# Optimization experiments

Hardware: AMD Instinct MI355X
Metric: run time of the kernel (lower is better)

## Reference

```python
import jax, jax.numpy as jnp
import numpy as np

N, E, G = 50000, 1600000, 64          # nodes, edges, graphs
NODE_IN, EDGE_IN, HID, L, H = 32, 16, 64, 3, 4
C = HID // H                           # per-head channels (PyG out_channels)


def setup_inputs() -> dict:
    key = jax.random.key(0)
    ks = jax.random.split(key, 12)
    x = jax.random.normal(ks[0], (N, NODE_IN), jnp.float32)
    edge_index = jax.random.randint(ks[1], (2, E), 0, N, jnp.int32)
    edge_attr = jax.random.normal(ks[2], (E, EDGE_IN), jnp.float32)
    batch = jnp.sort(jax.random.randint(ks[3], (N,), 0, G, jnp.int32))
    s = lambda k, shape, fan: jax.random.normal(k, shape, jnp.float32) / np.sqrt(fan)
    Wn = s(ks[4], (NODE_IN, HID), NODE_IN); bn = jnp.zeros((HID,), jnp.float32)
    Wq = s(ks[5], (L, HID, HID), HID);      bq = jnp.zeros((L, HID), jnp.float32)
    Wk = s(ks[6], (L, HID, HID), HID);      bk = jnp.zeros((L, HID), jnp.float32)
    Wv = s(ks[7], (L, HID, HID), HID);      bv = jnp.zeros((L, HID), jnp.float32)
    We = s(ks[8], (L, EDGE_IN, HID), EDGE_IN)          # lin_edge, bias=False in PyG
    Ws = s(ks[9], (L, HID, HID), HID);      bs = jnp.zeros((L, HID), jnp.float32)  # lin_skip
    W1 = s(ks[10], (HID, HID // 2), HID);   b1 = jnp.zeros((HID // 2,), jnp.float32)
    W2 = s(ks[11], (HID // 2, 1), HID // 2); b2 = jnp.zeros((1,), jnp.float32)
    return dict(x=x, edge_index=edge_index, edge_attr=edge_attr, batch=batch,
                Wn=Wn, bn=bn, Wq=Wq, bq=bq, Wk=Wk, bk=bk, Wv=Wv, bv=bv,
                We=We, Ws=Ws, bs=bs, W1=W1, b1=b1, W2=W2, b2=b2)


def _transformer_conv(x, src, dst, edge_attr, Wq, bq, Wk, bk, Wv, bv, We, Ws, bs):
    # PyG TransformerConv (concat=True, beta=False, root_weight=True), eval mode.
    q = (x @ Wq + bq)[dst].reshape(E, H, C)              # query at target nodes
    e = (edge_attr @ We).reshape(E, H, C)                # edge embedding
    k = (x @ Wk + bk)[src].reshape(E, H, C) + e          # key at source + edge
    alpha = (q * k).sum(-1) / jnp.sqrt(jnp.float32(C))   # [E, H]
    amax = jax.ops.segment_max(alpha, dst, num_segments=N)
    ex = jnp.exp(alpha - amax[dst])
    denom = jax.ops.segment_sum(ex, dst, num_segments=N)
    attn = ex / (denom[dst] + 1e-16)                     # segment softmax over in-edges
    v = (x @ Wv + bv)[src].reshape(E, H, C) + e
    agg = jax.ops.segment_sum((v * attn[..., None]).reshape(E, HID), dst, num_segments=N)
    return agg + x @ Ws + bs                             # skip connection (lin_skip)


def reference(x, edge_index, edge_attr, batch, Wn, bn, Wq, bq, Wk, bk, Wv, bv,
              We, Ws, bs, W1, b1, W2, b2):
    src, dst = edge_index[0], edge_index[1]
    h = jax.nn.relu(x @ Wn + bn)
    for l in range(L):  # dropout is identity in eval mode
        h_new = jax.nn.relu(_transformer_conv(h, src, dst, edge_attr,
                                              Wq[l], bq[l], Wk[l], bk[l],
                                              Wv[l], bv[l], We[l], Ws[l], bs[l]))
        h = h + h_new
    # global_mean_pool
    cnt = jax.ops.segment_sum(jnp.ones((N,), h.dtype), batch, num_segments=G)
    pooled = jax.ops.segment_sum(h, batch, num_segments=G) / jnp.maximum(cnt, 1.0)[:, None]
    out = jax.nn.relu(pooled @ W1 + b1) @ W2 + b2
    return out.squeeze(-1)
```

## Files before the change

### kernel.cpp

```cpp
#include <hip/hip_runtime.h>
#include <hip/hip_fp16.h>
#include <stdint.h>

#define Nn 50000
#define Ee 1600000
#define Gg 64
#define TB 2048
#define NTB ((Ee + TB - 1) / TB)
#define NBK ((Nn + 255) / 256)

typedef _Float16 f16x2 __attribute__((ext_vector_type(2)));
typedef _Float16 f16x4 __attribute__((ext_vector_type(4)));

__device__ __forceinline__ float fdot2f(f16x2 a, f16x2 b, float c) {
#if __has_builtin(__builtin_amdgcn_fdot2)
    return __builtin_amdgcn_fdot2(a, b, c, false);
#else
    return fmaf((float)a[0], (float)b[0], fmaf((float)a[1], (float)b[1], c));
#endif
}

__global__ void k_hist(const int* __restrict__ ei, int* __restrict__ deg) {
    int e = blockIdx.x * blockDim.x + threadIdx.x;
    if (e < Ee) atomicAdd(&deg[ei[Ee + e]], 1);
}

__global__ void k_scan1(const int* __restrict__ deg, int* __restrict__ row_ptr,
                        int* __restrict__ bsum) {
    __shared__ int buf[256];
    int i = blockIdx.x * 256 + threadIdx.x;
    int v = (i < Nn) ? deg[i] : 0;
    buf[threadIdx.x] = v;
    __syncthreads();
    for (int off = 1; off < 256; off <<= 1) {
        int t = (threadIdx.x >= off) ? buf[threadIdx.x - off] : 0;
        __syncthreads();
        buf[threadIdx.x] += t;
        __syncthreads();
    }
    if (i < Nn) row_ptr[i + 1] = buf[threadIdx.x];
    if (threadIdx.x == 255) bsum[blockIdx.x] = buf[255];
}

__global__ void k_scan2(int* __restrict__ bsum, int nb) {
    __shared__ int buf[256];
    int v = (threadIdx.x < nb) ? bsum[threadIdx.x] : 0;
    buf[threadIdx.x] = v;
    __syncthreads();
    for (int off = 1; off < 256; off <<= 1) {
        int t = (threadIdx.x >= off) ? buf[threadIdx.x - off] : 0;
        __syncthreads();
        buf[threadIdx.x] += t;
        __syncthreads();
    }
    if (threadIdx.x < nb) bsum[threadIdx.x] = buf[threadIdx.x];
}

__global__ void k_scan3(int* __restrict__ row_ptr, const int* __restrict__ bsum) {
    int i = blockIdx.x * 256 + threadIdx.x;
    if (i > Nn) return;
    if (i == 0) { row_ptr[0] = 0; return; }
    int b = (i - 1) >> 8;
    if (b > 0) row_ptr[i] += bsum[b - 1];
}

__global__ void k_scatter(const int* __restrict__ ei, int* __restrict__ cursor,
                          int* __restrict__ src_perm, int* __restrict__ eperm) {
    int e = blockIdx.x * blockDim.x + threadIdx.x;
    if (e >= Ee) return;
    int dst = ei[Ee + e];
    int pos = atomicAdd(&cursor[dst], 1);
    src_perm[pos] = ei[e];
    eperm[pos] = e;
}

__global__ void k_easort(const float* __restrict__ ea, const int* __restrict__ eperm,
                         __half* __restrict__ ea_h) {
    long t = (long)blockIdx.x * blockDim.x + threadIdx.x;
    if (t >= (long)Ee * 4) return;
    long idx = t >> 2;
    int e = eperm[idx];
    float4 v = ((const float4*)ea)[(long)e * 4 + (t & 3)];
    __half2 lo = __floats2half2_rn(v.x, v.y);
    __half2 hi = __floats2half2_rn(v.z, v.w);
    ((__half2*)ea_h)[t * 2]     = lo;
    ((__half2*)ea_h)[t * 2 + 1] = hi;
}


__global__ __launch_bounds__(256) void k_cnt(const int* __restrict__ ei,
                                             int* __restrict__ table) {
    __shared__ int hist[NBK];
    for (int i = threadIdx.x; i < NBK; i += 256) hist[i] = 0;
    __syncthreads();
    int e0 = blockIdx.x * TB;
    for (int i = threadIdx.x; i < TB; i += 256) {
        int e = e0 + i;
        if (e >= Ee) break;
        atomicAdd(&hist[ei[Ee + e] >> 8], 1);
    }
    __syncthreads();
    for (int i = threadIdx.x; i < NBK; i += 256)
        table[i * NTB + blockIdx.x] = hist[i];
}

__global__ __launch_bounds__(256) void k_colscan(int* __restrict__ table,
                                                 int* __restrict__ bktsz) {
    __shared__ int buf[1024];
    int c = blockIdx.x;
    for (int k = 0; k < 4; ++k) {
        int i = threadIdx.x + k * 256;
        buf[i] = (i < NTB) ? table[c * NTB + i] : 0;
    }
    __syncthreads();
    for (int off = 1; off < 1024; off <<= 1) {
        int v[4];
        for (int k = 0; k < 4; ++k) {
            int i = threadIdx.x + k * 256;
            v[k] = (i >= off) ? buf[i - off] : 0;
        }
        __syncthreads();
        for (int k = 0; k < 4; ++k) buf[threadIdx.x + k * 256] += v[k];
        __syncthreads();
    }
    for (int k = 0; k < 4; ++k) {
        int i = threadIdx.x + k * 256;
        if (i < NTB) table[c * NTB + i] = i ? buf[i - 1] : 0;
    }
    if (threadIdx.x == 0) bktsz[c] = buf[1023];
}

__global__ __launch_bounds__(256) void k_bktscan(const int* __restrict__ bktsz,
                                                 int* __restrict__ bktbase) {
    __shared__ int buf[256];
    int i = threadIdx.x;
    buf[i] = (i < NBK) ? bktsz[i] : 0;
    __syncthreads();
    for (int off = 1; off < 256; off <<= 1) {
        int v = (i >= off) ? buf[i - off] : 0;
        __syncthreads();
        buf[i] += v;
        __syncthreads();
    }
    if (i == 0) bktbase[0] = 0;
    if (i < NBK) bktbase[i + 1] = buf[i];
}

__global__ __launch_bounds__(256) void k_binfill(const int* __restrict__ ei,
                        const int* __restrict__ table, const int* __restrict__ bktbase,
                        unsigned long long* __restrict__ tmp) {
    __shared__ int off_s[NBK];
    __shared__ int cnt_s[NBK];
    for (int i = threadIdx.x; i < NBK; i += 256) {
        off_s[i] = table[i * NTB + blockIdx.x];
        cnt_s[i] = 0;
    }
    __syncthreads();
    int e0 = blockIdx.x * TB;
    for (int i = threadIdx.x; i < TB; i += 256) {
        int e = e0 + i;
        if (e >= Ee) break;
        int src = ei[e];
        int dst = ei[Ee + e];
        int b = dst >> 8;
        int r = atomicAdd(&cnt_s[b], 1);
        long pos = (long)bktbase[b] + off_s[b] + r;
        tmp[pos] = ((unsigned long long)(unsigned)dst << 37)
                 | ((unsigned long long)(unsigned)src << 21)
                 | (unsigned long long)(unsigned)e;
    }
}

__global__ __launch_bounds__(256) void k_bktB(const unsigned long long* __restrict__ tmp,
                        const int* __restrict__ bktbase, int* __restrict__ row_ptr,
                        unsigned long long* __restrict__ tmp2) {
    __shared__ int cnt[256];
    __shared__ int sc[256];
    __shared__ int lro[256];
    int b = blockIdx.x, tid = threadIdx.x;
    cnt[tid] = 0;
    __syncthreads();
    int s = bktbase[b], t_end = bktbase[b + 1];
    for (int i = s + tid; i < t_end; i += 256)
        atomicAdd(&cnt[(int)(tmp[i] >> 37) & 255], 1);
    __syncthreads();
    sc[tid] = cnt[tid];
    __syncthreads();
    for (int off = 1; off < 256; off <<= 1) {
        int v = (tid >= off) ? sc[tid - off] : 0;
        __syncthreads();
        sc[tid] += v;
        __syncthreads();
    }
    lro[tid] = tid ? sc[tid - 1] : 0;
    cnt[tid] = 0;
    int n = b * 256 + tid;
    if (n < Nn) row_ptr[n] = s + lro[tid];
    if (b == NBK - 1 && tid == 0) row_ptr[Nn] = Ee;
    __syncthreads();
    for (int i = s + tid; i < t_end; i += 256) {
        unsigned long long p = tmp[i];
        int dn = (int)(p >> 37) & 255;
        int r = atomicAdd(&cnt[dn], 1);
        int pos = s + lro[dn] + r;
        tmp2[pos] = (((p >> 21) & 0xFFFFull) << 32) | (p & 0x1FFFFFull);
    }
}

__global__ void k_scatB(const unsigned long long* __restrict__ tmp2,
                        int* __restrict__ src_perm,
                        const float* __restrict__ ea, __half* __restrict__ ea_h) {
    int t = blockIdx.x * blockDim.x + threadIdx.x;
    if (t >= Ee) return;
    unsigned long long p = tmp2[t];
    src_perm[t] = (int)(p >> 32);
    int e = (int)(p & 0xFFFFFFFFull);
    const float4* er = (const float4*)(ea + (size_t)e * 16);
    float4 v0 = er[0], v1 = er[1], v2 = er[2], v3 = er[3];
    __half2 h0 = __floats2half2_rn(v0.x, v0.y), h1 = __floats2half2_rn(v0.z, v0.w);
    __half2 h2 = __floats2half2_rn(v1.x, v1.y), h3 = __floats2half2_rn(v1.z, v1.w);
    __half2 h4 = __floats2half2_rn(v2.x, v2.y), h5 = __floats2half2_rn(v2.z, v2.w);
    __half2 h6 = __floats2half2_rn(v3.x, v3.y), h7 = __floats2half2_rn(v3.z, v3.w);
    uint4 a = make_uint4(*(unsigned*)&h0, *(unsigned*)&h1,
                         *(unsigned*)&h2, *(unsigned*)&h3);
    uint4 bb = make_uint4(*(unsigned*)&h4, *(unsigned*)&h5,
                          *(unsigned*)&h6, *(unsigned*)&h7);
    uint4* o = (uint4*)(ea_h + (size_t)t * 16);
    o[0] = a;
    o[1] = bb;
}

__global__ void k_gbound(const int* __restrict__ batch, int* __restrict__ gstart) {
    int n = blockIdx.x * blockDim.x + threadIdx.x;
    if (n >= Nn) return;
    int b = batch[n];
    if (n == 0) { for (int g = 0; g <= b; ++g) gstart[g] = 0; }
    else { int bp = batch[n - 1]; for (int g = bp + 1; g <= b; ++g) gstart[g] = n; }
    if (n == Nn - 1) { for (int g = b + 1; g <= Gg; ++g) gstart[g] = Nn; }
}

__global__ __launch_bounds__(256) void k_encode(const float* __restrict__ x,
                         const float* __restrict__ Wn,
                         const float* __restrict__ bn, float* __restrict__ h) {
    __shared__ float sx[64 * 32];
    int base = blockIdx.x * 64;
    for (int i = threadIdx.x; i < 512; i += 256) {
        int off = i * 4, row = off >> 5;
        float4 v = (base + row < Nn) ? ((const float4*)(x))[(base * 32 + off) >> 2]
                                     : make_float4(0.f, 0.f, 0.f, 0.f);
        ((float4*)sx)[i] = v;
    }
    __syncthreads();
    int lane = threadIdx.x & 63, wv = threadIdx.x >> 6;
    float acc[16];
    float b = bn[lane];
#pragma unroll
    for (int nn = 0; nn < 16; ++nn) acc[nn] = b;
#pragma unroll 1
    for (int k0 = 0; k0 < 32; k0 += 4) {
        float w0 = Wn[(k0 + 0) * 64 + lane];
        float w1 = Wn[(k0 + 1) * 64 + lane];
        float w2 = Wn[(k0 + 2) * 64 + lane];
        float w3 = Wn[(k0 + 3) * 64 + lane];
#pragma unroll
        for (int nn = 0; nn < 16; ++nn) {
            int row = wv * 16 + nn;
            float4 hv = *(const float4*)&sx[row * 32 + k0];
            acc[nn] = fmaf(hv.x, w0, fmaf(hv.y, w1, fmaf(hv.z, w2, fmaf(hv.w, w3, acc[nn]))));
        }
    }
#pragma unroll
    for (int nn = 0; nn < 16; ++nn) {
        int n = base + wv * 16 + nn;
        if (n < Nn) h[(size_t)n * 64 + lane] = fmaxf(acc[nn], 0.f);
    }
}

__global__ void k_wqm3(const float* __restrict__ Wq_all, const float* __restrict__ bq_all,
                       const float* __restrict__ We_all, float* __restrict__ Wqm3,
                       float* __restrict__ bqm3) {
    int l = blockIdx.x;
    const float* Wq = Wq_all + l * 4096;
    const float* bq = bq_all + l * 64;
    const float* We = We_all + l * 1024;
    float* Wqm = Wqm3 + l * 4096;
    float* bqm = bqm3 + l * 64;
    for (int o = threadIdx.x; o < 64 * 64; o += 256) {
        int j = o >> 6, lp = o & 63, hh = lp >> 4, ii = lp & 15;
        float acc = 0.f;
#pragma unroll
        for (int c = 0; c < 16; ++c)
            acc += Wq[j * 64 + hh * 16 + c] * We[ii * 64 + hh * 16 + c];
        Wqm[o] = acc;
    }
    if (threadIdx.x < 64) {
        int hh = threadIdx.x >> 4, ii = threadIdx.x & 15;
        float acc = 0.f;
#pragma unroll
        for (int c = 0; c < 16; ++c)
            acc += bq[hh * 16 + c] * We[ii * 64 + hh * 16 + c];
        bqm[threadIdx.x] = acc;
    }
}

__global__ void k_pack(const float* __restrict__ Wq, const float* __restrict__ Wk,
                       const float* __restrict__ Wv, const float* __restrict__ Wqm3,
                       const float* __restrict__ Ws, __half* __restrict__ pw) {
    int l = blockIdx.x / 5, m = blockIdx.x % 5;
    const float SC = 0.25f * 1.4426950408889634f;
    const float* src;
    float sc = 1.f;
    if (m == 0)      { src = Wq + l * 4096;   sc = SC; }
    else if (m == 1) { src = Wk + l * 4096; }
    else if (m == 2) { src = Wv + l * 4096; }
    else if (m == 3) { src = Wqm3 + l * 4096; sc = SC; }
    else             { src = Ws + l * 4096; }
    __half* dst = pw + ((size_t)l * 5 + m) * 4096;
    for (int i = threadIdx.x; i < 4096; i += 256) {
        int k = i >> 6, c = i & 63;
        dst[(k >> 1) * 128 + 2 * c + (k & 1)] = __float2half_rn(src[i] * sc);
    }
}

__global__ __launch_bounds__(256) void k_qkvt2(const float* __restrict__ h,
                       const __half* __restrict__ pw,
                       const float* __restrict__ bq, const float* __restrict__ bk,
                       const float* __restrict__ bv, const float* __restrict__ bqm,
                       const float* __restrict__ bs,
                       __half* __restrict__ qn16, __half* __restrict__ kv,
                       __half* __restrict__ tq16, float* __restrict__ sn) {
    __shared__ __half sh[64 * 64];
    int base = blockIdx.x * 64;
    for (int i = threadIdx.x; i < 1024; i += 256) {
        int off = i * 4, row = off >> 6;
        float4 v = (base + row < Nn) ? ((const float4*)(h))[((size_t)base * 64 + off) >> 2]
                                     : make_float4(0.f, 0.f, 0.f, 0.f);
        ((__half2*)sh)[i * 2]     = __floats2half2_rn(v.x, v.y);
        ((__half2*)sh)[i * 2 + 1] = __floats2half2_rn(v.z, v.w);
    }
    __syncthreads();
    int lane = threadIdx.x & 63, wv = threadIdx.x >> 6;
    const float SC = 0.25f * 1.4426950408889634f;
    const __half* Pq = pw;
    const __half* Pk = pw + 4096;
    const __half* Pv = pw + 8192;
    const __half* Pt = pw + 12288;
    const __half* Ps = pw + 16384;
    float aq[16], ak[16], av[16], at[16], as_[16];
    float _bq = bq[lane] * SC, _bk = bk[lane], _bv = bv[lane],
          _bt = bqm[lane] * SC, _bs = bs[lane];
#pragma unroll
    for (int nn = 0; nn < 16; ++nn) {
        aq[nn] = _bq; ak[nn] = _bk; av[nn] = _bv; at[nn] = _bt; as_[nn] = _bs;
    }
#pragma unroll 1
    for (int k0 = 0; k0 < 64; k0 += 4) {
        int pi = (k0 >> 1) * 128 + 2 * lane;
        f16x2 wq0 = *(const f16x2*)(Pq + pi), wq1 = *(const f16x2*)(Pq + pi + 128);
        f16x2 wk0 = *(const f16x2*)(Pk + pi), wk1 = *(const f16x2*)(Pk + pi + 128);
        f16x2 wv0 = *(const f16x2*)(Pv + pi), wv1 = *(const f16x2*)(Pv + pi + 128);
        f16x2 wt0 = *(const f16x2*)(Pt + pi), wt1 = *(const f16x2*)(Pt + pi + 128);
        f16x2 ws0 = *(const f16x2*)(Ps + pi), ws1 = *(const f16x2*)(Ps + pi + 128);
#pragma unroll
        for (int nn = 0; nn < 16; ++nn) {
            int row = wv * 16 + nn;
            f16x4 hv = *(const f16x4*)&sh[row * 64 + k0];
            f16x2 h01 = __builtin_shufflevector(hv, hv, 0, 1);
            f16x2 h23 = __builtin_shufflevector(hv, hv, 2, 3);
            aq[nn]  = fdot2f(h01, wq0, fdot2f(h23, wq1, aq[nn]));
            ak[nn]  = fdot2f(h01, wk0, fdot2f(h23, wk1, ak[nn]));
            av[nn]  = fdot2f(h01, wv0, fdot2f(h23, wv1, av[nn]));
            at[nn]  = fdot2f(h01, wt0, fdot2f(h23, wt1, at[nn]));
            as_[nn] = fdot2f(h01, ws0, fdot2f(h23, ws1, as_[nn]));
        }
    }
#pragma unroll
    for (int nn = 0; nn < 16; ++nn) {
        int n = base + wv * 16 + nn;
        if (n < Nn) {
            size_t o = (size_t)n * 64 + lane;
            qn16[o] = __float2half_rn(aq[nn]);
            tq16[o] = __float2half_rn(at[nn]);
            sn[o] = as_[nn];
            kv[(size_t)n * 128 + lane]      = __float2half_rn(ak[nn]);
            kv[(size_t)n * 128 + 64 + lane] = __float2half_rn(av[nn]);
        }
    }
}

__global__ __launch_bounds__(256) void k_layer5(float* __restrict__ h,
                      const __half* __restrict__ qn16, const __half* __restrict__ kv,
                      const __half* __restrict__ tq16, const float* __restrict__ sn,
                      const int* __restrict__ row_ptr, const int* __restrict__ src_perm,
                      const __half* __restrict__ eah, const float* __restrict__ We) {
    __shared__ float sWe[1024];
    __shared__ float tE[4][64];
    __shared__ float tV[4][64];
    for (int t = threadIdx.x; t < 1024; t += 256) sWe[t] = We[t];
    __syncthreads();
    int lane = threadIdx.x & 63, wv = threadIdx.x >> 6;
    int slot = lane >> 4, sl = lane & 15;
    int hh = lane >> 4;
    const int xoff = 4 * (sl & 3);
#pragma unroll 1
    for (int j = 0; j < 4; ++j) {
        int n = blockIdx.x * 16 + wv * 4 + j;
        if (n >= Nn) break;
        int beg = row_ptr[n], end = row_ptr[n + 1];
        f16x4 qv = *(const f16x4*)(qn16 + (size_t)n * 64 + 4 * sl);
        f16x4 tv = *(const f16x4*)(tq16 + (size_t)n * 64 + 4 * sl);
        f16x2 qa = __builtin_shufflevector(qv, qv, 0, 1);
        f16x2 qb = __builtin_shufflevector(qv, qv, 2, 3);
        f16x2 ta = __builtin_shufflevector(tv, tv, 0, 1);
        f16x2 tb = __builtin_shufflevector(tv, tv, 2, 3);
        float accd = 0.f;
        float4 accv = make_float4(0.f, 0.f, 0.f, 0.f);
        float4 acce = make_float4(0.f, 0.f, 0.f, 0.f);
        for (int idx = beg; idx < end; idx += 8) {
            int e0 = idx + slot, e1 = idx + 4 + slot;
            bool ok0 = e0 < end, ok1 = e1 < end;
            int i0 = ok0 ? e0 : beg, i1 = ok1 ? e1 : beg;
            int s0 = src_perm[i0], s1 = src_perm[i1];
            f16x4 k0 = *(const f16x4*)(kv + (size_t)s0 * 128 + 4 * sl);
            f16x4 v0 = *(const f16x4*)(kv + (size_t)s0 * 128 + 64 + 4 * sl);
            f16x4 k1 = *(const f16x4*)(kv + (size_t)s1 * 128 + 4 * sl);
            f16x4 v1 = *(const f16x4*)(kv + (size_t)s1 * 128 + 64 + 4 * sl);
            f16x4 x0 = *(const f16x4*)(eah + (size_t)i0 * 16 + xoff);
            f16x4 x1 = *(const f16x4*)(eah + (size_t)i1 * 16 + xoff);
            float a0 = fdot2f(qa, __builtin_shufflevector(k0, k0, 0, 1),
                       fdot2f(qb, __builtin_shufflevector(k0, k0, 2, 3),
                       fdot2f(ta, __builtin_shufflevector(x0, x0, 0, 1),
                       fdot2f(tb, __builtin_shufflevector(x0, x0, 2, 3), -6.0f))));
            float a1 = fdot2f(qa, __builtin_shufflevector(k1, k1, 0, 1),
                       fdot2f(qb, __builtin_shufflevector(k1, k1, 2, 3),
                       fdot2f(ta, __builtin_shufflevector(x1, x1, 0, 1),
                       fdot2f(tb, __builtin_shufflevector(x1, x1, 2, 3), -6.0f))));
            a0 += __shfl_xor(a0, 1, 4); a1 += __shfl_xor(a1, 1, 4);
            a0 += __shfl_xor(a0, 2, 4); a1 += __shfl_xor(a1, 2, 4);
            float p0 = ok0 ? __builtin_exp2f(a0) : 0.f;
            float p1 = ok1 ? __builtin_exp2f(a1) : 0.f;
            accd += p0 + p1;
            accv.x = fmaf(p0, (float)v0[0], fmaf(p1, (float)v1[0], accv.x));
            accv.y = fmaf(p0, (float)v0[1], fmaf(p1, (float)v1[1], accv.y));
            accv.z = fmaf(p0, (float)v0[2], fmaf(p1, (float)v1[2], accv.z));
            accv.w = fmaf(p0, (float)v0[3], fmaf(p1, (float)v1[3], accv.w));
            acce.x = fmaf(p0, (float)x0[0], fmaf(p1, (float)x1[0], acce.x));
            acce.y = fmaf(p0, (float)x0[1], fmaf(p1, (float)x1[1], acce.y));
            acce.z = fmaf(p0, (float)x0[2], fmaf(p1, (float)x1[2], acce.z));
            acce.w = fmaf(p0, (float)x0[3], fmaf(p1, (float)x1[3], acce.w));
        }
        accd   += __shfl_xor(accd, 16);   accd   += __shfl_xor(accd, 32);
        accv.x += __shfl_xor(accv.x, 16); accv.x += __shfl_xor(accv.x, 32);
        accv.y += __shfl_xor(accv.y, 16); accv.y += __shfl_xor(accv.y, 32);
        accv.z += __shfl_xor(accv.z, 16); accv.z += __shfl_xor(accv.z, 32);
        accv.w += __shfl_xor(accv.w, 16); accv.w += __shfl_xor(accv.w, 32);
        acce.x += __shfl_xor(acce.x, 16); acce.x += __shfl_xor(acce.x, 32);
        acce.y += __shfl_xor(acce.y, 16); acce.y += __shfl_xor(acce.y, 32);
        acce.z += __shfl_xor(acce.z, 16); acce.z += __shfl_xor(acce.z, 32);
        acce.w += __shfl_xor(acce.w, 16); acce.w += __shfl_xor(acce.w, 32);
        float inv = 1.f / (accd + 1e-16f);
        if (slot == 0) {
            ((float4*)tE[wv])[sl] = make_float4(acce.x * inv, acce.y * inv,
                                                acce.z * inv, acce.w * inv);
            ((float4*)tV[wv])[sl] = make_float4(accv.x * inv, accv.y * inv,
                                                accv.z * inv, accv.w * inv);
        }
        float re = 0.f;
#pragma unroll
        for (int i = 0; i < 16; ++i)
            re = fmaf(tE[wv][hh * 16 + i], sWe[i * 64 + lane], re);
        size_t o = (size_t)n * 64 + lane;
        float hv = h[o];
        h[o] = hv + fmaxf(tV[wv][lane] + re + sn[o], 0.f);
    }
}

__global__ __launch_bounds__(256) void k_layer(float* __restrict__ h,
                      const __half* __restrict__ qn16, const __half* __restrict__ kv,
                      const __half* __restrict__ tq16, const float* __restrict__ sn,
                      const int* __restrict__ row_ptr, const int* __restrict__ src_perm,
                      const int* __restrict__ eperm, const float* __restrict__ eaf,
                      const float* __restrict__ We) {
    __shared__ float sWe[1024];
    __shared__ float tile[4][64];
    for (int t = threadIdx.x; t < 1024; t += 256) sWe[t] = We[t];
    __syncthreads();
    int lane = threadIdx.x & 63, wv = threadIdx.x >> 6;
    int hh = lane >> 4, cc = lane & 15;
    int n = blockIdx.x * 4 + wv;
    if (n >= Nn) return;
    int beg = row_ptr[n], end = row_ptr[n + 1];
    float q = __half2float(qn16[(size_t)n * 64 + lane]);
    float t = __half2float(tq16[(size_t)n * 64 + lane]);
    float m = -INFINITY, accd = 0.f, accv = 0.f, acce = 0.f;
    int idx = beg;
    for (; idx < end; ++idx) {
        long b0 = (long)src_perm[idx] * 128;
        float k0 = __half2float(kv[b0 + lane]);
        float v0 = __half2float(kv[b0 + 64 + lane]);
        float x0 = eaf[(long)eperm[idx] * 16 + cc];
        float a0 = fmaf(q, k0, x0 * t);
        a0 += __shfl_xor(a0, 1, 16);
        a0 += __shfl_xor(a0, 2, 16);
        a0 += __shfl_xor(a0, 4, 16);
        a0 += __shfl_xor(a0, 8, 16);
        float nm = fmaxf(m, a0);
        float w = __builtin_exp2f(m - nm);
        float p0 = __builtin_exp2f(a0 - nm);
        accd = fmaf(accd, w, p0);
        accv = fmaf(accv, w, p0 * v0);
        acce = fmaf(acce, w, p0 * x0);
        m = nm;
    }
    float inv = 1.f / (accd + 1e-16f);
    tile[wv][lane] = acce * inv;
    float re = 0.f;
#pragma unroll
    for (int i = 0; i < 16; ++i)
        re = fmaf(tile[wv][hh * 16 + i], sWe[i * 64 + lane], re);
    size_t o = (size_t)n * 64 + lane;
    float hv = h[o];
    h[o] = hv + fmaxf(fmaf(accv, inv, re + sn[o]), 0.f);
}

__global__ void k_pool(const float* __restrict__ h, const int* __restrict__ gstart,
                       const float* __restrict__ W1, const float* __restrict__ b1,
                       const float* __restrict__ W2, const float* __restrict__ b2,
                       float* __restrict__ out) {
    int g = blockIdx.x;
    int lane = threadIdx.x & 63, wv = threadIdx.x >> 6;
    int beg = gstart[g], end = gstart[g + 1];
    __shared__ float red[4][64];
    __shared__ float sp[64];
    __shared__ float sh[32];
    float acc = 0.f;
    for (int n = beg + wv; n < end; n += 4) acc += h[(size_t)n * 64 + lane];
    red[wv][lane] = acc;
    __syncthreads();
    if (threadIdx.x < 64) {
        float c = fmaxf((float)(end - beg), 1.f);
        sp[lane] = (red[0][lane] + red[1][lane] + red[2][lane] + red[3][lane]) / c;
    }
    __syncthreads();
    if (threadIdx.x < 32) {
        int t = threadIdx.x;
        float a = b1[t];
#pragma unroll
        for (int i = 0; i < 64; ++i) a = fmaf(sp[i], W1[i * 32 + t], a);
        sh[t] = fmaxf(a, 0.f) * W2[t];
    }
    __syncthreads();
    if (threadIdx.x == 0) {
        float s = b2[0];
#pragma unroll
        for (int i = 0; i < 32; ++i) s += sh[i];
        out[g] = s;
    }
}

extern "C" void kernel_launch(void* const* d_in, const int* in_sizes, int n_in,
                              void* d_out, int out_size, void* d_ws, size_t ws_size,
                              hipStream_t stream) {
    const float* x   = (const float*)d_in[0];
    const int*   ei  = (const int*)d_in[1];
    const float* ea  = (const float*)d_in[2];
    const int*   bat = (const int*)d_in[3];
    const float* Wn  = (const float*)d_in[4];
    const float* bn  = (const float*)d_in[5];
    const float* Wq  = (const float*)d_in[6];
    const float* bq  = (const float*)d_in[7];
    const float* Wk  = (const float*)d_in[8];
    const float* bk  = (const float*)d_in[9];
    const float* Wv  = (const float*)d_in[10];
    const float* bv  = (const float*)d_in[11];
    const float* We  = (const float*)d_in[12];
    const float* Wsk = (const float*)d_in[13];
    const float* bs  = (const float*)d_in[14];
    const float* W1  = (const float*)d_in[15];
    const float* b1  = (const float*)d_in[16];
    const float* W2  = (const float*)d_in[17];
    const float* b2  = (const float*)d_in[18];
    float* out = (float*)d_out;

    const size_t NH = (size_t)Nn * 64;
    float* h    = (float*)d_ws;
    float* qn   = h + NH;
    float* tq   = h + 2 * NH;
    float* sn   = h + 3 * NH;
    __half* kv  = (__half*)(h + 4 * NH);
    float* Wqm3 = h + 5 * NH;
    float* bqm3 = Wqm3 + 3 * 4096;
    __half* pw  = (__half*)(bqm3 + 3 * 64);
    int* deg       = (int*)(pw + 3 * 5 * 4096);
    int* row_ptr   = deg + Nn;
    int* cursor    = row_ptr + Nn + 1;
    int* src_perm  = cursor + Nn;
    int* eperm     = src_perm + Ee;
    int* bsum      = eperm + Ee;
    int* gstart    = bsum + 256;
    char* pe = (char*)(gstart + Gg + 1);
    __half* ea_h = (__half*)(((uintptr_t)pe + 63) & ~(uintptr_t)63);
    char* pt = (char*)(ea_h + (size_t)Ee * 16);
    unsigned long long* tmp =
        (unsigned long long*)(((uintptr_t)pt + 15) & ~(uintptr_t)15);
    size_t need_eah = ((char*)(ea_h + (size_t)Ee * 16)) - (char*)d_ws;
    size_t need_tmp = ((char*)(tmp + Ee)) - (char*)d_ws;
    unsigned long long* tmp2 = (unsigned long long*)qn;
    int* table   = (int*)tq;
    int* bktsz   = (int*)sn;
    int* bktbase = bktsz + 256;
    __half* qn16 = (__half*)qn;
    __half* tq16 = (__half*)tq;
    int mode = (ws_size >= need_tmp) ? 2 : (ws_size >= need_eah) ? 1 : 0;

    if (mode == 2) {
        k_cnt<<<NTB, 256, 0, stream>>>(ei, table);
        k_colscan<<<NBK, 256, 0, stream>>>(table, bktsz);
        k_bktscan<<<1, 256, 0, stream>>>(bktsz, bktbase);
        k_binfill<<<NTB, 256, 0, stream>>>(ei, table, bktbase, tmp);
        k_bktB<<<NBK, 256, 0, stream>>>(tmp, bktbase, row_ptr, tmp2);
        k_scatB<<<(Ee + 255) / 256, 256, 0, stream>>>(tmp2, src_perm, ea, ea_h);
    } else {
        const int NB = 196;
        hipMemsetAsync(deg, 0, Nn * sizeof(int), stream);
        k_hist<<<(Ee + 255) / 256, 256, 0, stream>>>(ei, deg);
        k_scan1<<<NB, 256, 0, stream>>>(deg, row_ptr, bsum);
        k_scan2<<<1, 256, 0, stream>>>(bsum, NB);
        k_scan3<<<(Nn + 256) / 256, 256, 0, stream>>>(row_ptr, bsum);
        hipMemcpyAsync(cursor, row_ptr, Nn * sizeof(int), hipMemcpyDeviceToDevice, stream);
        k_scatter<<<(Ee + 255) / 256, 256, 0, stream>>>(ei, cursor, src_perm, eperm);
        if (mode == 1)
            k_easort<<<((long)Ee * 4 + 255) / 256, 256, 0, stream>>>(ea, eperm, ea_h);
    }
    k_gbound<<<(Nn + 255) / 256, 256, 0, stream>>>(bat, gstart);
    k_wqm3<<<3, 256, 0, stream>>>(Wq, bq, We, Wqm3, bqm3);
    k_pack<<<15, 256, 0, stream>>>(Wq, Wk, Wv, Wqm3, Wsk, pw);

    int nodeBlocks = (Nn + 63) / 64;
    k_encode<<<nodeBlocks, 256, 0, stream>>>(x, Wn, bn, h);
    for (int l = 0; l < 3; ++l) {
        k_qkvt2<<<nodeBlocks, 256, 0, stream>>>(h, pw + (size_t)l * 5 * 4096,
                                                bq + l * 64, bk + l * 64, bv + l * 64,
                                                bqm3 + l * 64, bs + l * 64,
                                                qn16, kv, tq16, sn);
        if (mode >= 1)
            k_layer5<<<(Nn + 15) / 16, 256, 0, stream>>>(h, qn16, kv, tq16, sn,
                    row_ptr, src_perm, ea_h, We + l * 1024);
        else
            k_layer<<<(Nn + 3) / 4, 256, 0, stream>>>(h, qn16, kv, tq16, sn,
                    row_ptr, src_perm, eperm, ea, We + l * 1024);
    }
    k_pool<<<Gg, 256, 0, stream>>>(h, gstart, W1, b1, W2, b2, out);
}
```

Measured before the change: 655.6 us.

## Interleave K/V per node, split edge sort output, use nontemporal edge-attr loads

K and V projections are now stored interleaved per node, so each 4-channel group of K sits next to the matching V group. The edge aggregation kernel can then fetch both with a single 16-byte gather per source instead of two 8-byte gathers. The bucket sort now writes src_perm and the original edge index directly, replacing the packed 64-bit intermediate. The edge-attr conversion kernel therefore reads only a 4-byte index and uses nontemporal loads for the streamed fp32 attributes. The per-edge K/V gather is the dominant random access, so halving its transaction count is the main aim.

```diff
diff --git a/kernel.cpp b/kernel.cpp
--- a/kernel.cpp
+++ b/kernel.cpp
@@ -11,6 +11,8 @@
 
 typedef _Float16 f16x2 __attribute__((ext_vector_type(2)));
 typedef _Float16 f16x4 __attribute__((ext_vector_type(4)));
+typedef _Float16 f16x8 __attribute__((ext_vector_type(8)));
+typedef float    f32x4v __attribute__((ext_vector_type(4)));
 
 __device__ __forceinline__ float fdot2f(f16x2 a, f16x2 b, float c) {
 #if __has_builtin(__builtin_amdgcn_fdot2)
@@ -173,7 +175,7 @@
 
 __global__ __launch_bounds__(256) void k_bktB(const unsigned long long* __restrict__ tmp,
                         const int* __restrict__ bktbase, int* __restrict__ row_ptr,
-                        unsigned long long* __restrict__ tmp2) {
+                        int* __restrict__ src_perm, int* __restrict__ eord) {
     __shared__ int cnt[256];
     __shared__ int sc[256];
     __shared__ int lro[256];
@@ -203,24 +205,25 @@
         int dn = (int)(p >> 37) & 255;
         int r = atomicAdd(&cnt[dn], 1);
         int pos = s + lro[dn] + r;
-        tmp2[pos] = (((p >> 21) & 0xFFFFull) << 32) | (p & 0x1FFFFFull);
-    }
-}
-
-__global__ void k_scatB(const unsigned long long* __restrict__ tmp2,
-                        int* __restrict__ src_perm,
-                        const float* __restrict__ ea, __half* __restrict__ ea_h) {
+        src_perm[pos] = (int)((p >> 21) & 0xFFFFull);
+        eord[pos] = (int)(p & 0x1FFFFFull);
+    }
+}
+
+__global__ void k_scatB2(const int* __restrict__ eord,
+                         const float* __restrict__ ea, __half* __restrict__ ea_h) {
     int t = blockIdx.x * blockDim.x + threadIdx.x;
     if (t >= Ee) return;
-    unsigned long long p = tmp2[t];
-    src_perm[t] = (int)(p >> 32);
-    int e = (int)(p & 0xFFFFFFFFull);
-    const float4* er = (const float4*)(ea + (size_t)e * 16);
-    float4 v0 = er[0], v1 = er[1], v2 = er[2], v3 = er[3];
-    __half2 h0 = __floats2half2_rn(v0.x, v0.y), h1 = __floats2half2_rn(v0.z, v0.w);
-    __half2 h2 = __floats2half2_rn(v1.x, v1.y), h3 = __floats2half2_rn(v1.z, v1.w);
-    __half2 h4 = __floats2half2_rn(v2.x, v2.y), h5 = __floats2half2_rn(v2.z, v2.w);
-    __half2 h6 = __floats2half2_rn(v3.x, v3.y), h7 = __floats2half2_rn(v3.z, v3.w);
+    int e = eord[t];
+    const f32x4v* er = (const f32x4v*)(ea + (size_t)e * 16);
+    f32x4v v0 = __builtin_nontemporal_load(er);
+    f32x4v v1 = __builtin_nontemporal_load(er + 1);
+    f32x4v v2 = __builtin_nontemporal_load(er + 2);
+    f32x4v v3 = __builtin_nontemporal_load(er + 3);
+    __half2 h0 = __floats2half2_rn(v0[0], v0[1]), h1 = __floats2half2_rn(v0[2], v0[3]);
+    __half2 h2 = __floats2half2_rn(v1[0], v1[1]), h3 = __floats2half2_rn(v1[2], v1[3]);
+    __half2 h4 = __floats2half2_rn(v2[0], v2[1]), h5 = __floats2half2_rn(v2[2], v2[3]);
+    __half2 h6 = __floats2half2_rn(v3[0], v3[1]), h7 = __floats2half2_rn(v3[2], v3[3]);
     uint4 a = make_uint4(*(unsigned*)&h0, *(unsigned*)&h1,
                          *(unsigned*)&h2, *(unsigned*)&h3);
     uint4 bb = make_uint4(*(unsigned*)&h4, *(unsigned*)&h5,
@@ -327,7 +330,7 @@
                        const float* __restrict__ bq, const float* __restrict__ bk,
                        const float* __restrict__ bv, const float* __restrict__ bqm,
                        const float* __restrict__ bs,
-                       __half* __restrict__ qn16, __half* __restrict__ kv,
+                       __half* __restrict__ qn16, __half* __restrict__ kvi,
                        __half* __restrict__ tq16, float* __restrict__ sn) {
     __shared__ __half sh[64 * 64];
     int base = blockIdx.x * 64;
@@ -374,6 +377,7 @@
             as_[nn] = fdot2f(h01, ws0, fdot2f(h23, ws1, as_[nn]));
         }
     }
+    int ko = 8 * (lane >> 2) + (lane & 3);
 #pragma unroll
     for (int nn = 0; nn < 16; ++nn) {
         int n = base + wv * 16 + nn;
@@ -382,14 +386,14 @@
             qn16[o] = __float2half_rn(aq[nn]);
             tq16[o] = __float2half_rn(at[nn]);
             sn[o] = as_[nn];
-            kv[(size_t)n * 128 + lane]      = __float2half_rn(ak[nn]);
-            kv[(size_t)n * 128 + 64 + lane] = __float2half_rn(av[nn]);
+            kvi[(size_t)n * 128 + ko]     = __float2half_rn(ak[nn]);
+            kvi[(size_t)n * 128 + ko + 4] = __float2half_rn(av[nn]);
         }
     }
 }
 
-__global__ __launch_bounds__(256) void k_layer5(float* __restrict__ h,
-                      const __half* __restrict__ qn16, const __half* __restrict__ kv,
+__global__ __launch_bounds__(256) void k_layer8(float* __restrict__ h,
+                      const __half* __restrict__ qn16, const __half* __restrict__ kvi,
                       const __half* __restrict__ tq16, const float* __restrict__ sn,
                       const int* __restrict__ row_ptr, const int* __restrict__ src_perm,
                       const __half* __restrict__ eah, const float* __restrict__ We) {
@@ -421,18 +425,16 @@
             bool ok0 = e0 < end, ok1 = e1 < end;
             int i0 = ok0 ? e0 : beg, i1 = ok1 ? e1 : beg;
             int s0 = src_perm[i0], s1 = src_perm[i1];
-            f16x4 k0 = *(const f16x4*)(kv + (size_t)s0 * 128 + 4 * sl);
-            f16x4 v0 = *(const f16x4*)(kv + (size_t)s0 * 128 + 64 + 4 * sl);
-            f16x4 k1 = *(const f16x4*)(kv + (size_t)s1 * 128 + 4 * sl);
-            f16x4 v1 = *(const f16x4*)(kv + (size_t)s1 * 128 + 64 + 4 * sl);
+            f16x8 kv0 = *(const f16x8*)(kvi + (size_t)s0 * 128 + 8 * sl);
+            f16x8 kv1 = *(const f16x8*)(kvi + (size_t)s1 * 128 + 8 * sl);
             f16x4 x0 = *(const f16x4*)(eah + (size_t)i0 * 16 + xoff);
             f16x4 x1 = *(const f16x4*)(eah + (size_t)i1 * 16 + xoff);
-            float a0 = fdot2f(qa, __builtin_shufflevector(k0, k0, 0, 1),
-                       fdot2f(qb, __builtin_shufflevector(k0, k0, 2, 3),
+            float a0 = fdot2f(qa, __builtin_shufflevector(kv0, kv0, 0, 1),
+                       fdot2f(qb, __builtin_shufflevector(kv0, kv0, 2, 3),
                        fdot2f(ta, __builtin_shufflevector(x0, x0, 0, 1),
                        fdot2f(tb, __builtin_shufflevector(x0, x0, 2, 3), -6.0f))));
-            float a1 = fdot2f(qa, __builtin_shufflevector(k1, k1, 0, 1),
-                       fdot2f(qb, __builtin_shufflevector(k1, k1, 2, 3),
+            float a1 = fdot2f(qa, __builtin_shufflevector(kv1, kv1, 0, 1),
+                       fdot2f(qb, __builtin_shufflevector(kv1, kv1, 2, 3),
                        fdot2f(ta, __builtin_shufflevector(x1, x1, 0, 1),
                        fdot2f(tb, __builtin_shufflevector(x1, x1, 2, 3), -6.0f))));
             a0 += __shfl_xor(a0, 1, 4); a1 += __shfl_xor(a1, 1, 4);
@@ -440,10 +442,10 @@
             float p0 = ok0 ? __builtin_exp2f(a0) : 0.f;
             float p1 = ok1 ? __builtin_exp2f(a1) : 0.f;
             accd += p0 + p1;
-            accv.x = fmaf(p0, (float)v0[0], fmaf(p1, (float)v1[0], accv.x));
-            accv.y = fmaf(p0, (float)v0[1], fmaf(p1, (float)v1[1], accv.y));
-            accv.z = fmaf(p0, (float)v0[2], fmaf(p1, (float)v1[2], accv.z));
-            accv.w = fmaf(p0, (float)v0[3], fmaf(p1, (float)v1[3], accv.w));
+            accv.x = fmaf(p0, (float)kv0[4], fmaf(p1, (float)kv1[4], accv.x));
+            accv.y = fmaf(p0, (float)kv0[5], fmaf(p1, (float)kv1[5], accv.y));
+            accv.z = fmaf(p0, (float)kv0[6], fmaf(p1, (float)kv1[6], accv.z));
+            accv.w = fmaf(p0, (float)kv0[7], fmaf(p1, (float)kv1[7], accv.w));
             acce.x = fmaf(p0, (float)x0[0], fmaf(p1, (float)x1[0], acce.x));
             acce.y = fmaf(p0, (float)x0[1], fmaf(p1, (float)x1[1], acce.y));
             acce.z = fmaf(p0, (float)x0[2], fmaf(p1, (float)x1[2], acce.z));
@@ -476,7 +478,7 @@
 }
 
 __global__ __launch_bounds__(256) void k_layer(float* __restrict__ h,
-                      const __half* __restrict__ qn16, const __half* __restrict__ kv,
+                      const __half* __restrict__ qn16, const __half* __restrict__ kvi,
                       const __half* __restrict__ tq16, const float* __restrict__ sn,
                       const int* __restrict__ row_ptr, const int* __restrict__ src_perm,
                       const int* __restrict__ eperm, const float* __restrict__ eaf,
@@ -487,6 +489,7 @@
     __syncthreads();
     int lane = threadIdx.x & 63, wv = threadIdx.x >> 6;
     int hh = lane >> 4, cc = lane & 15;
+    int ko = 8 * (lane >> 2) + (lane & 3);
     int n = blockIdx.x * 4 + wv;
     if (n >= Nn) return;
     int beg = row_ptr[n], end = row_ptr[n + 1];
@@ -496,8 +499,8 @@
     int idx = beg;
     for (; idx < end; ++idx) {
         long b0 = (long)src_perm[idx] * 128;
-        float k0 = __half2float(kv[b0 + lane]);
-        float v0 = __half2float(kv[b0 + 64 + lane]);
+        float k0 = __half2float(kvi[b0 + ko]);
+        float v0 = __half2float(kvi[b0 + ko + 4]);
         float x0 = eaf[(long)eperm[idx] * 16 + cc];
         float a0 = fmaf(q, k0, x0 * t);
         a0 += __shfl_xor(a0, 1, 16);
@@ -605,7 +608,7 @@
         (unsigned long long*)(((uintptr_t)pt + 15) & ~(uintptr_t)15);
     size_t need_eah = ((char*)(ea_h + (size_t)Ee * 16)) - (char*)d_ws;
     size_t need_tmp = ((char*)(tmp + Ee)) - (char*)d_ws;
-    unsigned long long* tmp2 = (unsigned long long*)qn;
+    int* eord    = (int*)qn;
     int* table   = (int*)tq;
     int* bktsz   = (int*)sn;
     int* bktbase = bktsz + 256;
@@ -618,8 +621,8 @@
         k_colscan<<<NBK, 256, 0, stream>>>(table, bktsz);
         k_bktscan<<<1, 256, 0, stream>>>(bktsz, bktbase);
         k_binfill<<<NTB, 256, 0, stream>>>(ei, table, bktbase, tmp);
-        k_bktB<<<NBK, 256, 0, stream>>>(tmp, bktbase, row_ptr, tmp2);
-        k_scatB<<<(Ee + 255) / 256, 256, 0, stream>>>(tmp2, src_perm, ea, ea_h);
+        k_bktB<<<NBK, 256, 0, stream>>>(tmp, bktbase, row_ptr, src_perm, eord);
+        k_scatB2<<<(Ee + 255) / 256, 256, 0, stream>>>(eord, ea, ea_h);
     } else {
         const int NB = 196;
         hipMemsetAsync(deg, 0, Nn * sizeof(int), stream);
@@ -644,7 +647,7 @@
                                                 bqm3 + l * 64, bs + l * 64,
                                                 qn16, kv, tq16, sn);
         if (mode >= 1)
-            k_layer5<<<(Nn + 15) / 16, 256, 0, stream>>>(h, qn16, kv, tq16, sn,
+            k_layer8<<<(Nn + 15) / 16, 256, 0, stream>>>(h, qn16, kv, tq16, sn,
                     row_ptr, src_perm, ea_h, We + l * 1024);
         else
             k_layer<<<(Nn + 3) / 4, 256, 0, stream>>>(h, qn16, kv, tq16, sn,
```

After: 683.5 us. +4.3%, slower.
